# Performance work log

Measured on AMD Instinct MI355X. Metric: run time of the kernel, lower is better.

## Reference

```python
import jax, jax.numpy as jnp
import numpy as np

N, F_IN, HID, HEADS, NCLS, E = 50000, 512, 64, 4, 64, 800000
NEG_SLOPE = 0.2
EPS = 1e-16


def setup_inputs() -> dict:
    key = jax.random.key(0)
    ks = jax.random.split(key, 10)
    s = 0.1
    return {
        "x": jax.random.normal(ks[0], (N, F_IN), jnp.float32),
        "edge_index": jax.random.randint(ks[1], (2, E), 0, N, jnp.int64),
        "W1": jax.random.normal(ks[2], (F_IN, HEADS * HID), jnp.float32) * s,
        "a_src1": jax.random.normal(ks[3], (HEADS, HID), jnp.float32) * s,
        "a_dst1": jax.random.normal(ks[4], (HEADS, HID), jnp.float32) * s,
        "b1": jax.random.normal(ks[5], (HEADS * HID,), jnp.float32) * s,
        "W2": jax.random.normal(ks[6], (HEADS * HID, NCLS), jnp.float32) * s,
        "a_src2": jax.random.normal(ks[7], (1, NCLS), jnp.float32) * s,
        "a_dst2": jax.random.normal(ks[8], (1, NCLS), jnp.float32) * s,
        "b2": jax.random.normal(ks[9], (NCLS,), jnp.float32) * s,
    }


def gat_conv(x, W, a_src, a_dst, b, src, dst):
    H, C = a_src.shape
    h = (x @ W).reshape(-1, H, C)                     # [N, H, C]
    # per-node attention halves, gathered per edge -> [E', H]
    al_src = jnp.einsum("nhc,hc->nh", h, a_src)
    al_dst = jnp.einsum("nhc,hc->nh", h, a_dst)
    e = jax.nn.leaky_relu(al_src[src] + al_dst[dst], NEG_SLOPE)
    # segment softmax over destination neighborhoods
    m = jax.ops.segment_max(e, dst, num_segments=x.shape[0])
    ex = jnp.exp(e - m[dst])
    denom = jax.ops.segment_sum(ex, dst, num_segments=x.shape[0])
    alpha = ex / (denom[dst] + EPS)                   # [E', H]
    out = jax.ops.segment_sum(alpha[:, :, None] * h[src], dst,
                              num_segments=x.shape[0])  # [N, H, C]
    return out.reshape(-1, H * C) + b


def reference(x, edge_index, W1, a_src1, a_dst1, b1, W2, a_src2, a_dst2, b2):
    n = x.shape[0]
    loop = jnp.arange(n, dtype=edge_index.dtype)
    src = jnp.concatenate([edge_index[0], loop])       # add self loops (PyG default)
    dst = jnp.concatenate([edge_index[1], loop])
    h = gat_conv(x, W1, a_src1, a_dst1, b1, src, dst)
    h = jax.nn.elu(h)                                  # dropout is identity in eval
    out = gat_conv(h, W2, a_src2, a_dst2, b2, src, dst)
    return jax.nn.log_softmax(out, axis=1)
```

## Files before the change

### kernel.cpp

```cpp
#include <hip/hip_runtime.h>
#include <math.h>

#define F_IN 512
#define HC1 256
#define HEADS 4
#define HID 64
#define NCLS 64
#define NEG_SLOPE 0.2f
#define EPS_DENOM 1e-16f

using short8 = __attribute__((ext_vector_type(8))) short;
using f32x4  = __attribute__((ext_vector_type(4))) float;

__device__ inline float wave_sum(float v) {
#pragma unroll
  for (int s = 32; s > 0; s >>= 1) v += __shfl_xor(v, s);
  return v;
}
__device__ inline float wave_max(float v) {
#pragma unroll
  for (int s = 32; s > 0; s >>= 1) v = fmaxf(v, __shfl_xor(v, s));
  return v;
}

__device__ inline unsigned short f2bf(float f) {
  unsigned int u = __float_as_uint(f);
  u = (u + 0x7FFF + ((u >> 16) & 1)) >> 16;
  return (unsigned short)u;
}
__device__ inline float bflo(unsigned int u) { return __uint_as_float(u << 16); }
__device__ inline float bfhi(unsigned int u) { return __uint_as_float(u & 0xFFFF0000u); }

__device__ inline unsigned int cvtpk_bf16(float lo, float hi) {
  unsigned int r;
  asm("v_cvt_pk_bf16_f32 %0, %1, %2" : "=v"(r) : "v"(lo), "v"(hi));
  return r;
}

__device__ inline void async_copy16(const void* g, void* l) {
  __builtin_amdgcn_global_load_lds((const __attribute__((address_space(1))) void*)g,
                                   (__attribute__((address_space(3))) void*)l, 16, 0, 0);
}

__global__ void castT_kernel(const float* __restrict__ W, unsigned short* __restrict__ WT,
                             int K, int Nn) {
  int id = blockIdx.x * blockDim.x + threadIdx.x;
  if (id >= K * Nn) return;
  int n = id / K, k = id % K;
  WT[id] = f2bf(W[(size_t)k * Nn + n]);
}


__global__ void hist_kernel(const int* __restrict__ dst, int E, int* __restrict__ cnt) {
  int i = blockIdx.x * blockDim.x + threadIdx.x;
  int stride = gridDim.x * blockDim.x;
  for (int e = i; e < E; e += stride) atomicAdd(&cnt[dst[e]], 1);
}

__global__ void scan_blocks_kernel(const int* __restrict__ cnt, int n,
                                   int* __restrict__ rowoff, int* __restrict__ cursor,
                                   int* __restrict__ bsum) {
  __shared__ int wpart[16];
  int b = blockIdx.x, tid = threadIdx.x;
  int i = b * 1024 + tid;
  int lane = tid & 63, wid = tid >> 6;
  int v = (i < n) ? (cnt[i] + 1) : 0;
  int x = v;
#pragma unroll
  for (int s = 1; s < 64; s <<= 1) {
    int t = __shfl_up(x, s);
    if (lane >= s) x += t;
  }
  if (lane == 63) wpart[wid] = x;
  __syncthreads();
  if (wid == 0) {
    int p = (lane < 16) ? wpart[lane] : 0;
#pragma unroll
    for (int s = 1; s < 16; s <<= 1) {
      int t = __shfl_up(p, s);
      if (lane >= s) p += t;
    }
    if (lane < 16) wpart[lane] = p;
  }
  __syncthreads();
  int incl = x + (wid ? wpart[wid - 1] : 0);
  if (i < n) { rowoff[i + 1] = incl; cursor[i] = incl - v; }
  if (tid == 1023) bsum[b] = incl;
  if (b == 0 && tid == 0) rowoff[0] = 0;
}

__global__ void scan_partials_kernel(int* __restrict__ bsum, int nb) {
  int lane = threadIdx.x;
  int v = (lane < nb) ? bsum[lane] : 0;
  int x = v;
#pragma unroll
  for (int s = 1; s < 64; s <<= 1) {
    int t = __shfl_up(x, s);
    if (lane >= s) x += t;
  }
  if (lane < nb) bsum[lane] = x - v;
}

__global__ void scan_add_kernel(int n, int* __restrict__ rowoff, int* __restrict__ cursor,
                                const int* __restrict__ bsum) {
  int i = blockIdx.x * 1024 + threadIdx.x;
  int off = bsum[blockIdx.x];
  if (i < n) { rowoff[i + 1] += off; cursor[i] += off; }
}

__global__ void scatter_kernel(const int* __restrict__ src, const int* __restrict__ dst,
                               int E, int n, int* __restrict__ cursor, int* __restrict__ esrc) {
  int i = blockIdx.x * blockDim.x + threadIdx.x;
  int stride = gridDim.x * blockDim.x;
  for (int e = i; e < E + n; e += stride) {
    int s, d;
    if (e < E) { s = src[e]; d = dst[e]; } else { s = e - E; d = s; }
    int pos = atomicAdd(&cursor[d], 1);
    esrc[pos] = s;
  }
}


__global__ __launch_bounds__(256)
void gemm1_fused_kernel(const float* __restrict__ A, const unsigned short* __restrict__ BT,
                        unsigned short* __restrict__ Cb, int M) {
  constexpr int BM = 128, BN = 128, BK = 32, K = F_IN, Nn = HC1;
  __shared__ unsigned short Alds[BM * BK];
  __shared__ unsigned short Blds[BN * BK];
  const int t = threadIdx.x;
  const int lane = t & 63;
  const int w = t >> 6;
  const int wr = (w >> 1) * 64;
  const int wc = (w & 1) * 64;
  const int row0 = blockIdx.y * BM;
  const int col0 = blockIdx.x * BN;
  const int lrow = lane & 15;
  const int lk = (lane >> 4) * 8;

  f32x4 acc[4][4] = {};
  const int ar = t >> 1;
  const int kh = (t & 1) * 16;
  int grow = row0 + ar; if (grow > M - 1) grow = M - 1;
  const float* arow = A + (size_t)grow * K + kh;

  for (int k0 = 0; k0 < K; k0 += BK) {
#pragma unroll
    for (int i = 0; i < 2; ++i) {
      int c = i * 256 + t;
      int br = c >> 2;
      int bk = (c & 3) * 8;
      const unsigned short* g = BT + (size_t)(col0 + br) * K + k0 + bk;
      unsigned short* l = Blds + (size_t)(i * 256 + w * 64) * 8;
      async_copy16(g, l);
    }
    const float4* gp = (const float4*)(arow + k0);
    float4 f0 = gp[0], f1 = gp[1], f2 = gp[2], f3 = gp[3];
    uint4 u0, u1;
    u0.x = cvtpk_bf16(f0.x, f0.y); u0.y = cvtpk_bf16(f0.z, f0.w);
    u0.z = cvtpk_bf16(f1.x, f1.y); u0.w = cvtpk_bf16(f1.z, f1.w);
    u1.x = cvtpk_bf16(f2.x, f2.y); u1.y = cvtpk_bf16(f2.z, f2.w);
    u1.z = cvtpk_bf16(f3.x, f3.y); u1.w = cvtpk_bf16(f3.z, f3.w);
    uint4* dstp = (uint4*)&Alds[ar * BK + kh];
    dstp[0] = u0; dstp[1] = u1;
    __syncthreads();
    short8 a[4], b[4];
#pragma unroll
    for (int m = 0; m < 4; ++m)
      a[m] = *(const short8*)&Alds[(wr + m * 16 + lrow) * BK + lk];
#pragma unroll
    for (int n = 0; n < 4; ++n)
      b[n] = *(const short8*)&Blds[(wc + n * 16 + lrow) * BK + lk];
#pragma unroll
    for (int m = 0; m < 4; ++m)
#pragma unroll
      for (int n = 0; n < 4; ++n)
        acc[m][n] = __builtin_amdgcn_mfma_f32_16x16x32_bf16(a[m], b[n], acc[m][n], 0, 0, 0);
    __syncthreads();
  }
#pragma unroll
  for (int m = 0; m < 4; ++m) {
#pragma unroll
    for (int j = 0; j < 4; ++j) {
      int r = row0 + wr + m * 16 + (lane >> 4) * 4 + j;
      if (r < M) {
#pragma unroll
        for (int n = 0; n < 4; ++n)
          Cb[(size_t)r * Nn + col0 + wc + n * 16 + lrow] = f2bf(acc[m][n][j]);
      }
    }
  }
}


template <int BN>
__global__ __launch_bounds__(256)
void mfma_gemm_kernel(const unsigned short* __restrict__ A,
                      const unsigned short* __restrict__ BT,
                      unsigned short* __restrict__ Cb, int M, int Nn, int K) {
  constexpr int BM = 128, BK = 32;
  constexpr int NACC = BN / 32;
  __shared__ unsigned short Alds[BM * BK];
  __shared__ unsigned short Blds[BN * BK];
  const int t = threadIdx.x;
  const int lane = t & 63;
  const int w = t >> 6;
  const int wr = (w >> 1) * 64;
  const int wc = (w & 1) * (BN / 2);
  const int row0 = blockIdx.y * BM;
  const int col0 = blockIdx.x * BN;
  const int lrow = lane & 15;
  const int lk = (lane >> 4) * 8;

  f32x4 acc[4][NACC] = {};
  constexpr int AI = (BM * BK) / (256 * 8);
  constexpr int BI = (BN * BK) / (256 * 8);

  for (int k0 = 0; k0 < K; k0 += BK) {
#pragma unroll
    for (int i = 0; i < AI; ++i) {
      int c = i * 256 + t;
      int ar = c >> 2;
      int ak = (c & 3) * 8;
      int grow = row0 + ar; if (grow > M - 1) grow = M - 1;
      const unsigned short* g = A + (size_t)grow * K + k0 + ak;
      unsigned short* l = Alds + (size_t)(i * 256 + w * 64) * 8;
      async_copy16(g, l);
    }
#pragma unroll
    for (int i = 0; i < BI; ++i) {
      int c = i * 256 + t;
      int br = c >> 2;
      int bk = (c & 3) * 8;
      const unsigned short* g = BT + (size_t)(col0 + br) * K + k0 + bk;
      unsigned short* l = Blds + (size_t)(i * 256 + w * 64) * 8;
      async_copy16(g, l);
    }
    __syncthreads();
    short8 a[4], b[NACC];
#pragma unroll
    for (int m = 0; m < 4; ++m)
      a[m] = *(const short8*)&Alds[(wr + m * 16 + lrow) * BK + lk];
#pragma unroll
    for (int n = 0; n < NACC; ++n)
      b[n] = *(const short8*)&Blds[(wc + n * 16 + lrow) * BK + lk];
#pragma unroll
    for (int m = 0; m < 4; ++m)
#pragma unroll
      for (int n = 0; n < NACC; ++n)
        acc[m][n] = __builtin_amdgcn_mfma_f32_16x16x32_bf16(a[m], b[n], acc[m][n], 0, 0, 0);
    __syncthreads();
  }
#pragma unroll
  for (int m = 0; m < 4; ++m) {
#pragma unroll
    for (int j = 0; j < 4; ++j) {
      int r = row0 + wr + m * 16 + (lane >> 4) * 4 + j;
      if (r < M) {
#pragma unroll
        for (int n = 0; n < NACC; ++n)
          Cb[(size_t)r * Nn + col0 + wc + n * 16 + lrow] = f2bf(acc[m][n][j]);
      }
    }
  }
}


__global__ void attn1_kernel(const unsigned short* __restrict__ h1b,
                             const float* __restrict__ a_src, const float* __restrict__ a_dst,
                             float* __restrict__ als, float* __restrict__ ald, int n) {
  int w = threadIdx.x >> 6;
  int node = blockIdx.x * 4 + w;
  if (node >= n) return;
  int lane = threadIdx.x & 63;
  uint2 d = *(const uint2*)&h1b[(size_t)node * HC1 + lane * 4];
  float f0 = bflo(d.x), f1 = bfhi(d.x), f2 = bflo(d.y), f3 = bfhi(d.y);
  float4 as_ = ((const float4*)a_src)[lane];
  float4 ad_ = ((const float4*)a_dst)[lane];
  float ps = f0 * as_.x + f1 * as_.y + f2 * as_.z + f3 * as_.w;
  float pd = f0 * ad_.x + f1 * ad_.y + f2 * ad_.z + f3 * ad_.w;
#pragma unroll
  for (int s = 1; s < 16; s <<= 1) {
    ps += __shfl_xor(ps, s);
    pd += __shfl_xor(pd, s);
  }
  if ((lane & 15) == 0) {
    als[node * HEADS + (lane >> 4)] = ps;
    ald[node * HEADS + (lane >> 4)] = pd;
  }
}

__global__ void attn2_kernel(const unsigned short* __restrict__ h2b,
                             const float* __restrict__ a_src, const float* __restrict__ a_dst,
                             float* __restrict__ als, float* __restrict__ ald, int n) {
  int w = threadIdx.x >> 6;
  int node = blockIdx.x * 4 + w;
  if (node >= n) return;
  int lane = threadIdx.x & 63;
  float v = __uint_as_float(((unsigned int)h2b[(size_t)node * NCLS + lane]) << 16);
  float ps = wave_sum(v * a_src[lane]);
  float pd = wave_sum(v * a_dst[lane]);
  if (lane == 0) { als[node] = ps; ald[node] = pd; }
}


__global__ void agg1_kernel(const unsigned short* __restrict__ h1b,
                            const float4* __restrict__ als1, const float4* __restrict__ ald1,
                            const int* __restrict__ rowoff, const int* __restrict__ esrc,
                            const float* __restrict__ b1, unsigned short* __restrict__ hact,
                            int n) {
  __shared__ float wlds[4][256];
  __shared__ int   slds[4][64];
  int w = threadIdx.x >> 6;
  int node = blockIdx.x * 4 + w;
  if (node >= n) return;
  int lane = threadIdx.x & 63;
  int beg = rowoff[node], end = rowoff[node + 1];
  float4 aldn = ald1[node];
  int hsel = lane >> 4;
  float4 acc = {0.f, 0.f, 0.f, 0.f};
  float4 dl  = {0.f, 0.f, 0.f, 0.f};
  for (int base = beg; base < end; base += 64) {
    int cnt = min(64, end - base);
    int e = base + lane;
    if (e < end) {
      int s = esrc[e];
      float4 av = als1[s];
      float v, w0, w1, w2, w3;
      v = av.x + aldn.x; v = fmaxf(v, NEG_SLOPE * v); w0 = __expf(v);
      v = av.y + aldn.y; v = fmaxf(v, NEG_SLOPE * v); w1 = __expf(v);
      v = av.z + aldn.z; v = fmaxf(v, NEG_SLOPE * v); w2 = __expf(v);
      v = av.w + aldn.w; v = fmaxf(v, NEG_SLOPE * v); w3 = __expf(v);
      dl.x += w0; dl.y += w1; dl.z += w2; dl.w += w3;
      slds[w][lane] = s;
      float4 wv = {w0, w1, w2, w3};
      *(float4*)&wlds[w][lane * 4] = wv;
    }
    for (int j0 = 0; j0 < cnt; j0 += 8) {
      int g = cnt - j0;
      uint2 d[8]; float wj[8];
#pragma unroll
      for (int jj = 0; jj < 8; ++jj) {
        if (jj < g) {
          int ss = slds[w][j0 + jj];
          wj[jj] = wlds[w][(j0 + jj) * 4 + hsel];
          d[jj] = *(const uint2*)&h1b[(size_t)ss * HC1 + lane * 4];
        }
      }
#pragma unroll
      for (int jj = 0; jj < 8; ++jj) {
        if (jj < g) {
          acc.x += wj[jj] * bflo(d[jj].x);
          acc.y += wj[jj] * bfhi(d[jj].x);
          acc.z += wj[jj] * bflo(d[jj].y);
          acc.w += wj[jj] * bfhi(d[jj].y);
        }
      }
    }
  }
  float d0 = wave_sum(dl.x), d1 = wave_sum(dl.y);
  float d2 = wave_sum(dl.z), d3 = wave_sum(dl.w);
  float den = hsel < 2 ? (hsel == 0 ? d0 : d1) : (hsel == 2 ? d2 : d3);
  float rden = 1.f / (den + EPS_DENOM);
  float4 bv = ((const float4*)b1)[lane];
  float o0 = acc.x * rden + bv.x;
  float o1 = acc.y * rden + bv.y;
  float o2 = acc.z * rden + bv.z;
  float o3 = acc.w * rden + bv.w;
  o0 = o0 > 0.f ? o0 : __expf(o0) - 1.f;
  o1 = o1 > 0.f ? o1 : __expf(o1) - 1.f;
  o2 = o2 > 0.f ? o2 : __expf(o2) - 1.f;
  o3 = o3 > 0.f ? o3 : __expf(o3) - 1.f;
  ushort4 ov = {f2bf(o0), f2bf(o1), f2bf(o2), f2bf(o3)};
  *(ushort4*)&hact[(size_t)node * HC1 + lane * 4] = ov;
}

__global__ void agg2_kernel(const unsigned short* __restrict__ h2b,
                            const float* __restrict__ als2, const float* __restrict__ ald2,
                            const int* __restrict__ rowoff, const int* __restrict__ esrc,
                            const float* __restrict__ b2, float* __restrict__ out, int n) {
  __shared__ float wlds[4][64];
  __shared__ int   slds[4][64];
  int w = threadIdx.x >> 6;
  int node = blockIdx.x * 4 + w;
  if (node >= n) return;
  int lane = threadIdx.x & 63;
  int g16 = lane >> 4, c = lane & 15;
  int beg = rowoff[node], end = rowoff[node + 1];
  float aldn = ald2[node];
  float4 acc = {0.f, 0.f, 0.f, 0.f};
  float dl = 0.f;
  for (int base = beg; base < end; base += 64) {
    int cnt = min(64, end - base);
    int e = base + lane;
    if (e < end) {
      int s = esrc[e];
      float v = als2[s] + aldn;
      v = fmaxf(v, NEG_SLOPE * v);
      float wl = __expf(v);
      dl += wl;
      slds[w][lane] = s;
      wlds[w][lane] = wl;
    }
    for (int j0 = 0; j0 < cnt; j0 += 8) {
      int i0 = j0 + g16, i1 = j0 + 4 + g16;
      bool v0 = i0 < cnt, v1 = i1 < cnt;
      int ss0 = slds[w][v0 ? i0 : 0];
      int ss1 = slds[w][v1 ? i1 : 0];
      float w0 = wlds[w][v0 ? i0 : 0];
      float w1 = wlds[w][v1 ? i1 : 0];
      if (v0) {
        uint2 dd = *(const uint2*)&h2b[(size_t)ss0 * NCLS + c * 4];
        acc.x += w0 * bflo(dd.x); acc.y += w0 * bfhi(dd.x);
        acc.z += w0 * bflo(dd.y); acc.w += w0 * bfhi(dd.y);
      }
      if (v1) {
        uint2 dd = *(const uint2*)&h2b[(size_t)ss1 * NCLS + c * 4];
        acc.x += w1 * bflo(dd.x); acc.y += w1 * bfhi(dd.x);
        acc.z += w1 * bflo(dd.y); acc.w += w1 * bfhi(dd.y);
      }
    }
  }
#pragma unroll
  for (int s = 16; s < 64; s <<= 1) {
    acc.x += __shfl_xor(acc.x, s);
    acc.y += __shfl_xor(acc.y, s);
    acc.z += __shfl_xor(acc.z, s);
    acc.w += __shfl_xor(acc.w, s);
  }
  float den = wave_sum(dl);
  float rden = 1.f / (den + EPS_DENOM);
  float4 bv = *(const float4*)&b2[c * 4];
  float o0 = acc.x * rden + bv.x;
  float o1 = acc.y * rden + bv.y;
  float o2 = acc.z * rden + bv.z;
  float o3 = acc.w * rden + bv.w;
  float mx = fmaxf(fmaxf(o0, o1), fmaxf(o2, o3));
#pragma unroll
  for (int s = 1; s < 16; s <<= 1) mx = fmaxf(mx, __shfl_xor(mx, s));
  float sm = __expf(o0 - mx) + __expf(o1 - mx) + __expf(o2 - mx) + __expf(o3 - mx);
#pragma unroll
  for (int s = 1; s < 16; s <<= 1) sm += __shfl_xor(sm, s);
  float ls = mx + __logf(sm);
  if (g16 == 0) {
    float4 ov = {o0 - ls, o1 - ls, o2 - ls, o3 - ls};
    *(float4*)&out[(size_t)node * NCLS + c * 4] = ov;
  }
}


extern "C" void kernel_launch(void* const* d_in, const int* in_sizes, int n_in,
                              void* d_out, int out_size, void* d_ws, size_t ws_size,
                              hipStream_t stream) {
  const float* x      = (const float*)d_in[0];
  const int*   eidx   = (const int*)d_in[1];
  const float* W1     = (const float*)d_in[2];
  const float* a_src1 = (const float*)d_in[3];
  const float* a_dst1 = (const float*)d_in[4];
  const float* b1     = (const float*)d_in[5];
  const float* W2     = (const float*)d_in[6];
  const float* a_src2 = (const float*)d_in[7];
  const float* a_dst2 = (const float*)d_in[8];
  const float* b2     = (const float*)d_in[9];
  float* out = (float*)d_out;

  const int Nn = in_sizes[0] / F_IN;
  const int E  = in_sizes[1] / 2;
  const int* esrc_in = eidx;
  const int* edst_in = eidx + E;

  char* ws = (char*)d_ws;
  size_t off = 0;
  auto alloc = [&](size_t bytes) -> void* {
    void* p = ws + off;
    off += (bytes + 255) & ~(size_t)255;
    return p;
  };
  unsigned short* h1b    = (unsigned short*)alloc((size_t)Nn * HC1 * sizeof(short));
  unsigned short* hact   = (unsigned short*)alloc((size_t)Nn * HC1 * sizeof(short));
  unsigned short* h2b    = (unsigned short*)alloc((size_t)Nn * NCLS * sizeof(short));
  unsigned short* W1T    = (unsigned short*)alloc((size_t)F_IN * HC1 * sizeof(short));
  unsigned short* W2T    = (unsigned short*)alloc((size_t)HC1 * NCLS * sizeof(short));
  float*          als1   = (float*)alloc((size_t)Nn * HEADS * sizeof(float));
  float*          ald1   = (float*)alloc((size_t)Nn * HEADS * sizeof(float));
  float*          als2   = (float*)alloc((size_t)Nn * sizeof(float));
  float*          ald2   = (float*)alloc((size_t)Nn * sizeof(float));
  int*            cnt    = (int*)alloc((size_t)Nn * sizeof(int));
  int*            rowoff = (int*)alloc((size_t)(Nn + 1) * sizeof(int));
  int*            cursor = (int*)alloc((size_t)Nn * sizeof(int));
  int*            bsum   = (int*)alloc(256 * sizeof(int));
  int*            esrc   = (int*)alloc((size_t)(E + Nn) * sizeof(int));

  const int nscan = (Nn + 1023) / 1024;

  castT_kernel<<<(F_IN * HC1 + 255) / 256, 256, 0, stream>>>(W1, W1T, F_IN, HC1);
  castT_kernel<<<(HC1 * NCLS + 255) / 256, 256, 0, stream>>>(W2, W2T, HC1, NCLS);

  hipMemsetAsync(cnt, 0, (size_t)Nn * sizeof(int), stream);
  hist_kernel<<<(E + 255) / 256, 256, 0, stream>>>(edst_in, E, cnt);
  scan_blocks_kernel<<<nscan, 1024, 0, stream>>>(cnt, Nn, rowoff, cursor, bsum);
  scan_partials_kernel<<<1, 64, 0, stream>>>(bsum, nscan);
  scan_add_kernel<<<nscan, 1024, 0, stream>>>(Nn, rowoff, cursor, bsum);
  scatter_kernel<<<(E + Nn + 255) / 256, 256, 0, stream>>>(esrc_in, edst_in, E, Nn, cursor, esrc);

  {
    dim3 g(HC1 / 128, (Nn + 127) / 128);
    gemm1_fused_kernel<<<g, 256, 0, stream>>>(x, W1T, h1b, Nn);
  }
  {
    int blocks = (Nn + 3) / 4;
    attn1_kernel<<<blocks, 256, 0, stream>>>(h1b, a_src1, a_dst1, als1, ald1, Nn);
    agg1_kernel<<<blocks, 256, 0, stream>>>(h1b, (const float4*)als1, (const float4*)ald1,
                                            rowoff, esrc, b1, hact, Nn);
  }

  {
    dim3 g(NCLS / 64, (Nn + 127) / 128);
    mfma_gemm_kernel<64><<<g, 256, 0, stream>>>(hact, W2T, h2b, Nn, NCLS, HC1);
  }
  {
    int blocks = (Nn + 3) / 4;
    attn2_kernel<<<blocks, 256, 0, stream>>>(h2b, a_src2, a_dst2, als2, ald2, Nn);
    agg2_kernel<<<blocks, 256, 0, stream>>>(h2b, als2, ald2, rowoff, esrc, b2, out, Nn);
  }
}
```

Measured before the change: 286.2 us.

## Widen gathers to 16-byte loads and double-buffer neighbor fetches in aggregation kernels

In agg1 each lane now loads 8 bf16 values (uint4) instead of 4, so half-waves process two edges at once. The edge loop is restructured into a two-buffer issue/consume pipeline so the next batch of neighbor rows is in flight while the current one is accumulated. agg2 likewise uses uint4 loads with 8 lanes per row, handling 8 edges per step, and needs more cross-lane shuffle reductions at the end. This aims to cut the number of memory instructions and raise memory-level parallelism on the gather-bound aggregation, at the cost of more registers and extra reduction shuffles.

```diff
diff --git a/kernel.cpp b/kernel.cpp
--- a/kernel.cpp
+++ b/kernel.cpp
@@ -15,11 +15,6 @@
 __device__ inline float wave_sum(float v) {
 #pragma unroll
   for (int s = 32; s > 0; s >>= 1) v += __shfl_xor(v, s);
-  return v;
-}
-__device__ inline float wave_max(float v) {
-#pragma unroll
-  for (int s = 32; s > 0; s >>= 1) v = fmaxf(v, __shfl_xor(v, s));
   return v;
 }
 
@@ -314,64 +309,93 @@
   int node = blockIdx.x * 4 + w;
   if (node >= n) return;
   int lane = threadIdx.x & 63;
+  int hi = lane >> 5;
+  int cl = lane & 31;
+  int head = cl >> 3;
   int beg = rowoff[node], end = rowoff[node + 1];
   float4 aldn = ald1[node];
-  int hsel = lane >> 4;
-  float4 acc = {0.f, 0.f, 0.f, 0.f};
-  float4 dl  = {0.f, 0.f, 0.f, 0.f};
+  f32x4 accA = {0.f, 0.f, 0.f, 0.f};
+  f32x4 accB = {0.f, 0.f, 0.f, 0.f};
+  float dl0 = 0.f, dl1 = 0.f, dl2 = 0.f, dl3 = 0.f;
+
   for (int base = beg; base < end; base += 64) {
     int cnt = min(64, end - base);
-    int e = base + lane;
-    if (e < end) {
-      int s = esrc[e];
+    if (lane < cnt) {
+      int s = esrc[base + lane];
       float4 av = als1[s];
       float v, w0, w1, w2, w3;
       v = av.x + aldn.x; v = fmaxf(v, NEG_SLOPE * v); w0 = __expf(v);
       v = av.y + aldn.y; v = fmaxf(v, NEG_SLOPE * v); w1 = __expf(v);
       v = av.z + aldn.z; v = fmaxf(v, NEG_SLOPE * v); w2 = __expf(v);
       v = av.w + aldn.w; v = fmaxf(v, NEG_SLOPE * v); w3 = __expf(v);
-      dl.x += w0; dl.y += w1; dl.z += w2; dl.w += w3;
+      dl0 += w0; dl1 += w1; dl2 += w2; dl3 += w3;
       slds[w][lane] = s;
       float4 wv = {w0, w1, w2, w3};
       *(float4*)&wlds[w][lane * 4] = wv;
     }
-    for (int j0 = 0; j0 < cnt; j0 += 8) {
-      int g = cnt - j0;
-      uint2 d[8]; float wj[8];
-#pragma unroll
-      for (int jj = 0; jj < 8; ++jj) {
-        if (jj < g) {
-          int ss = slds[w][j0 + jj];
-          wj[jj] = wlds[w][(j0 + jj) * 4 + hsel];
-          d[jj] = *(const uint2*)&h1b[(size_t)ss * HC1 + lane * 4];
-        }
+
+    uint4 dA[4], dB[4];
+    float wA[4], wB[4];
+    auto ISSUE = [&](int j0, uint4* d, float* wj) {
+#pragma unroll
+      for (int ii = 0; ii < 4; ++ii) {
+        int e = j0 + 2 * ii + hi;
+        bool val = e < cnt;
+        int se = val ? e : 0;
+        int ss = slds[w][se];
+        wj[ii] = val ? wlds[w][se * 4 + head] : 0.f;
+        d[ii] = *(const uint4*)&h1b[(size_t)ss * HC1 + cl * 8];
       }
-#pragma unroll
-      for (int jj = 0; jj < 8; ++jj) {
-        if (jj < g) {
-          acc.x += wj[jj] * bflo(d[jj].x);
-          acc.y += wj[jj] * bfhi(d[jj].x);
-          acc.z += wj[jj] * bflo(d[jj].y);
-          acc.w += wj[jj] * bfhi(d[jj].y);
-        }
+    };
+    auto CONSUME = [&](const uint4* d, const float* wj) {
+#pragma unroll
+      for (int ii = 0; ii < 4; ++ii) {
+        float q = wj[ii];
+        accA[0] += q * bflo(d[ii].x); accA[1] += q * bfhi(d[ii].x);
+        accA[2] += q * bflo(d[ii].y); accA[3] += q * bfhi(d[ii].y);
+        accB[0] += q * bflo(d[ii].z); accB[1] += q * bfhi(d[ii].z);
+        accB[2] += q * bflo(d[ii].w); accB[3] += q * bfhi(d[ii].w);
       }
-    }
-  }
-  float d0 = wave_sum(dl.x), d1 = wave_sum(dl.y);
-  float d2 = wave_sum(dl.z), d3 = wave_sum(dl.w);
-  float den = hsel < 2 ? (hsel == 0 ? d0 : d1) : (hsel == 2 ? d2 : d3);
+    };
+
+    ISSUE(0, dA, wA);
+    for (int j0 = 8;; j0 += 16) {
+      bool hasB = j0 < cnt;
+      if (hasB) ISSUE(j0, dB, wB);
+      CONSUME(dA, wA);
+      if (!hasB) break;
+      bool hasA = (j0 + 8) < cnt;
+      if (hasA) ISSUE(j0 + 8, dA, wA);
+      CONSUME(dB, wB);
+      if (!hasA) break;
+    }
+  }
+
+#pragma unroll
+  for (int k = 0; k < 4; ++k) {
+    accA[k] += __shfl_xor(accA[k], 32);
+    accB[k] += __shfl_xor(accB[k], 32);
+  }
+  float d0 = wave_sum(dl0), d1 = wave_sum(dl1);
+  float d2 = wave_sum(dl2), d3 = wave_sum(dl3);
+  float den = head < 2 ? (head == 0 ? d0 : d1) : (head == 2 ? d2 : d3);
   float rden = 1.f / (den + EPS_DENOM);
-  float4 bv = ((const float4*)b1)[lane];
-  float o0 = acc.x * rden + bv.x;
-  float o1 = acc.y * rden + bv.y;
-  float o2 = acc.z * rden + bv.z;
-  float o3 = acc.w * rden + bv.w;
-  o0 = o0 > 0.f ? o0 : __expf(o0) - 1.f;
-  o1 = o1 > 0.f ? o1 : __expf(o1) - 1.f;
-  o2 = o2 > 0.f ? o2 : __expf(o2) - 1.f;
-  o3 = o3 > 0.f ? o3 : __expf(o3) - 1.f;
-  ushort4 ov = {f2bf(o0), f2bf(o1), f2bf(o2), f2bf(o3)};
-  *(ushort4*)&hact[(size_t)node * HC1 + lane * 4] = ov;
+  if (hi == 0) {
+    float4 bv0 = *(const float4*)&b1[cl * 8];
+    float4 bv1 = *(const float4*)&b1[cl * 8 + 4];
+    float o[8];
+    o[0] = accA[0] * rden + bv0.x; o[1] = accA[1] * rden + bv0.y;
+    o[2] = accA[2] * rden + bv0.z; o[3] = accA[3] * rden + bv0.w;
+    o[4] = accB[0] * rden + bv1.x; o[5] = accB[1] * rden + bv1.y;
+    o[6] = accB[2] * rden + bv1.z; o[7] = accB[3] * rden + bv1.w;
+    ushort4 ov0, ov1;
+#pragma unroll
+    for (int k = 0; k < 8; ++k) o[k] = o[k] > 0.f ? o[k] : __expf(o[k]) - 1.f;
+    ov0.x = f2bf(o[0]); ov0.y = f2bf(o[1]); ov0.z = f2bf(o[2]); ov0.w = f2bf(o[3]);
+    ov1.x = f2bf(o[4]); ov1.y = f2bf(o[5]); ov1.z = f2bf(o[6]); ov1.w = f2bf(o[7]);
+    *(ushort4*)&hact[(size_t)node * HC1 + cl * 8] = ov0;
+    *(ushort4*)&hact[(size_t)node * HC1 + cl * 8 + 4] = ov1;
+  }
 }
 
 __global__ void agg2_kernel(const unsigned short* __restrict__ h2b,
@@ -384,16 +408,17 @@
   int node = blockIdx.x * 4 + w;
   if (node >= n) return;
   int lane = threadIdx.x & 63;
-  int g16 = lane >> 4, c = lane & 15;
+  int eg = lane >> 3;
+  int cl = lane & 7;
   int beg = rowoff[node], end = rowoff[node + 1];
   float aldn = ald2[node];
-  float4 acc = {0.f, 0.f, 0.f, 0.f};
+  f32x4 accA = {0.f, 0.f, 0.f, 0.f};
+  f32x4 accB = {0.f, 0.f, 0.f, 0.f};
   float dl = 0.f;
   for (int base = beg; base < end; base += 64) {
     int cnt = min(64, end - base);
-    int e = base + lane;
-    if (e < end) {
-      int s = esrc[e];
+    if (lane < cnt) {
+      int s = esrc[base + lane];
       float v = als2[s] + aldn;
       v = fmaxf(v, NEG_SLOPE * v);
       float wl = __expf(v);
@@ -401,49 +426,60 @@
       slds[w][lane] = s;
       wlds[w][lane] = wl;
     }
-    for (int j0 = 0; j0 < cnt; j0 += 8) {
-      int i0 = j0 + g16, i1 = j0 + 4 + g16;
-      bool v0 = i0 < cnt, v1 = i1 < cnt;
-      int ss0 = slds[w][v0 ? i0 : 0];
-      int ss1 = slds[w][v1 ? i1 : 0];
-      float w0 = wlds[w][v0 ? i0 : 0];
-      float w1 = wlds[w][v1 ? i1 : 0];
-      if (v0) {
-        uint2 dd = *(const uint2*)&h2b[(size_t)ss0 * NCLS + c * 4];
-        acc.x += w0 * bflo(dd.x); acc.y += w0 * bfhi(dd.x);
-        acc.z += w0 * bflo(dd.y); acc.w += w0 * bfhi(dd.y);
+    for (int j0 = 0; j0 < cnt; j0 += 32) {
+      uint4 d[4]; float wj[4];
+#pragma unroll
+      for (int ii = 0; ii < 4; ++ii) {
+        int e = j0 + ii * 8 + eg;
+        bool val = e < cnt;
+        int se = val ? e : 0;
+        int ss = slds[w][se];
+        wj[ii] = val ? wlds[w][se] : 0.f;
+        d[ii] = *(const uint4*)&h2b[(size_t)ss * NCLS + cl * 8];
       }
-      if (v1) {
-        uint2 dd = *(const uint2*)&h2b[(size_t)ss1 * NCLS + c * 4];
-        acc.x += w1 * bflo(dd.x); acc.y += w1 * bfhi(dd.x);
-        acc.z += w1 * bflo(dd.y); acc.w += w1 * bfhi(dd.y);
+#pragma unroll
+      for (int ii = 0; ii < 4; ++ii) {
+        float q = wj[ii];
+        accA[0] += q * bflo(d[ii].x); accA[1] += q * bfhi(d[ii].x);
+        accA[2] += q * bflo(d[ii].y); accA[3] += q * bfhi(d[ii].y);
+        accB[0] += q * bflo(d[ii].z); accB[1] += q * bfhi(d[ii].z);
+        accB[2] += q * bflo(d[ii].w); accB[3] += q * bfhi(d[ii].w);
       }
     }
   }
 #pragma unroll
-  for (int s = 16; s < 64; s <<= 1) {
-    acc.x += __shfl_xor(acc.x, s);
-    acc.y += __shfl_xor(acc.y, s);
-    acc.z += __shfl_xor(acc.z, s);
-    acc.w += __shfl_xor(acc.w, s);
+  for (int s = 8; s < 64; s <<= 1) {
+#pragma unroll
+    for (int k = 0; k < 4; ++k) {
+      accA[k] += __shfl_xor(accA[k], s);
+      accB[k] += __shfl_xor(accB[k], s);
+    }
   }
   float den = wave_sum(dl);
   float rden = 1.f / (den + EPS_DENOM);
-  float4 bv = *(const float4*)&b2[c * 4];
-  float o0 = acc.x * rden + bv.x;
-  float o1 = acc.y * rden + bv.y;
-  float o2 = acc.z * rden + bv.z;
-  float o3 = acc.w * rden + bv.w;
-  float mx = fmaxf(fmaxf(o0, o1), fmaxf(o2, o3));
-#pragma unroll
-  for (int s = 1; s < 16; s <<= 1) mx = fmaxf(mx, __shfl_xor(mx, s));
-  float sm = __expf(o0 - mx) + __expf(o1 - mx) + __expf(o2 - mx) + __expf(o3 - mx);
-#pragma unroll
-  for (int s = 1; s < 16; s <<= 1) sm += __shfl_xor(sm, s);
+  float4 bv0 = *(const float4*)&b2[cl * 8];
+  float4 bv1 = *(const float4*)&b2[cl * 8 + 4];
+  float o[8];
+  o[0] = accA[0] * rden + bv0.x; o[1] = accA[1] * rden + bv0.y;
+  o[2] = accA[2] * rden + bv0.z; o[3] = accA[3] * rden + bv0.w;
+  o[4] = accB[0] * rden + bv1.x; o[5] = accB[1] * rden + bv1.y;
+  o[6] = accB[2] * rden + bv1.z; o[7] = accB[3] * rden + bv1.w;
+  float mx = o[0];
+#pragma unroll
+  for (int k = 1; k < 8; ++k) mx = fmaxf(mx, o[k]);
+#pragma unroll
+  for (int s = 1; s < 8; s <<= 1) mx = fmaxf(mx, __shfl_xor(mx, s));
+  float sm = 0.f;
+#pragma unroll
+  for (int k = 0; k < 8; ++k) sm += __expf(o[k] - mx);
+#pragma unroll
+  for (int s = 1; s < 8; s <<= 1) sm += __shfl_xor(sm, s);
   float ls = mx + __logf(sm);
-  if (g16 == 0) {
-    float4 ov = {o0 - ls, o1 - ls, o2 - ls, o3 - ls};
-    *(float4*)&out[(size_t)node * NCLS + c * 4] = ov;
+  if (lane < 8) {
+    float4 q0 = {o[0] - ls, o[1] - ls, o[2] - ls, o[3] - ls};
+    float4 q1 = {o[4] - ls, o[5] - ls, o[6] - ls, o[7] - ls};
+    *(float4*)&out[(size_t)node * NCLS + cl * 8] = q0;
+    *(float4*)&out[(size_t)node * NCLS + cl * 8 + 4] = q1;
   }
 }
 
```

New measurement: 279.5 us. 1.02x faster.
